# Kernel tuning notes

Hardware: AMD Instinct MI355X
Metric: run time of the kernel (lower is better)

The kernel has to match this reference:

```python
import jax, jax.numpy as jnp
import numpy as np

HIDDEN = 2048
NUM_EXPERTS = 64
TOP_K = 2


def setup_inputs() -> dict:
    key = jax.random.key(0)
    k1, k2 = jax.random.split(key)
    x = jax.random.normal(k1, (4, 4096, HIDDEN), dtype=jnp.float32)
    # nn.Linear(hidden, num_experts, bias=False): weight shape [E, H], y = x @ W.T
    W = jax.random.normal(k2, (NUM_EXPERTS, HIDDEN), dtype=jnp.float32) * (HIDDEN ** -0.5)
    return {"x": x, "W": W}


def reference(x, W):
    B, S, H = x.shape
    E, K = NUM_EXPERTS, TOP_K
    xf = x.reshape(-1, H)                       # [N, H]
    gate_logits = xf @ W.T                      # [N, E]
    routing_probs = jax.nn.softmax(gate_logits, axis=-1)
    top_k_probs, top_k_indices = jax.lax.top_k(routing_probs, K)  # [N, K]
    denom = jnp.sum(top_k_probs, axis=-1, keepdims=True) + 1e-6
    routing_weights = (top_k_probs / denom).reshape(B, S, K)
    expert_indices = top_k_indices.reshape(B, S, K)

    # aux load-balancing loss (training path)
    N = xf.shape[0]
    # expert_mask.mean(0): fraction of tokens assigned to each expert
    assign_per_expert = jnp.zeros((E,), jnp.float32).at[top_k_indices.reshape(-1)].add(1.0) / N
    prob_per_expert = jnp.mean(routing_probs, axis=0)             # [E]
    aux_loss = (jnp.sum(prob_per_expert * prob_per_expert) * E
                + jnp.sum(assign_per_expert * assign_per_expert) * E)

    # expert_counts update (bincount over selected indices)
    expert_counts = jnp.zeros((E,), jnp.float32).at[top_k_indices.reshape(-1)].add(1.0)

    return routing_weights, expert_indices, aux_loss, expert_counts
```

## Files before the change

### kernel.cpp

```cpp
#include <hip/hip_runtime.h>

#define HID 2048
#define NEXP 64
#define NTOK 16384
#define TM 64
#define BK 64
#define NTHREADS 256
#define NCHUNK (HID / BK)
#define RS 72
#define PLANE_B (64 * RS * 2)
#define CHUNK_B (3 * PLANE_B)
#define WS_W_OFF 1024

#define OUT_IDX_OFF (2 * NTOK)
#define OUT_AUX_OFF (4 * NTOK)
#define OUT_CNT_OFF (4 * NTOK + 1)

typedef __attribute__((ext_vector_type(8))) short bhalf8;
typedef __attribute__((ext_vector_type(4))) float f32x4;

__device__ __forceinline__ void split3(float v, unsigned short& h1, unsigned short& h2, unsigned short& h3) {
    unsigned int u = __float_as_uint(v);
    unsigned int r1 = (u + 0x7FFFu + ((u >> 16) & 1u)) & 0xFFFF0000u;
    float f1 = __uint_as_float(r1);
    float d1 = v - f1;
    unsigned int u2 = __float_as_uint(d1);
    unsigned int r2 = (u2 + 0x7FFFu + ((u2 >> 16) & 1u)) & 0xFFFF0000u;
    float f2 = __uint_as_float(r2);
    float d2 = d1 - f2;
    h1 = (unsigned short)(r1 >> 16);
    h2 = (unsigned short)(r2 >> 16);
    h3 = (unsigned short)(__float_as_uint(d2) >> 16);
}

__global__ __launch_bounds__(256) void wsplit_kernel(const float* __restrict__ W, char* __restrict__ wq) {
    int idx8 = (blockIdx.x * 256 + threadIdx.x) * 8;
    int e = idx8 >> 11;
    int kk = idx8 & 2047;
    int c = kk >> 6;
    int j = kk & 63;
    const float4* wp = (const float4*)(W + (size_t)e * HID + kk);
    float4 v0 = wp[0], v1 = wp[1];
    float f[8] = {v0.x, v0.y, v0.z, v0.w, v1.x, v1.y, v1.z, v1.w};
    unsigned int p1[4], p2[4], p3[4];
#pragma unroll
    for (int t = 0; t < 4; t++) {
        unsigned short a1, a2, a3, b1, b2, b3;
        split3(f[2 * t], a1, a2, a3);
        split3(f[2 * t + 1], b1, b2, b3);
        p1[t] = (unsigned int)a1 | ((unsigned int)b1 << 16);
        p2[t] = (unsigned int)a2 | ((unsigned int)b2 << 16);
        p3[t] = (unsigned int)a3 | ((unsigned int)b3 << 16);
    }
    char* base = wq + (size_t)c * CHUNK_B + e * (RS * 2) + j * 2;
    *(uint4*)(base)               = make_uint4(p1[0], p1[1], p1[2], p1[3]);
    *(uint4*)(base + PLANE_B)     = make_uint4(p2[0], p2[1], p2[2], p2[3]);
    *(uint4*)(base + 2 * PLANE_B) = make_uint4(p3[0], p3[1], p3[2], p3[3]);
}

__device__ __forceinline__ void load_x_slot(const float* __restrict__ x, int n0, int c, int s,
                                            float4& a, float4& b) {
    int row = s >> 3, oct = s & 7;
    const float4* gp = (const float4*)(x + (size_t)(n0 + row) * HID + c * BK + oct * 8);
    a = gp[0];
    b = gp[1];
}

__device__ __forceinline__ void conv_store_x(char* xpl, int s, float4 a, float4 b) {
    int row = s >> 3, oct = s & 7;
    float f[8] = {a.x, a.y, a.z, a.w, b.x, b.y, b.z, b.w};
    unsigned int p1[4], p2[4], p3[4];
#pragma unroll
    for (int t = 0; t < 4; t++) {
        unsigned short a1, a2, a3, b1, b2, b3;
        split3(f[2 * t], a1, a2, a3);
        split3(f[2 * t + 1], b1, b2, b3);
        p1[t] = (unsigned int)a1 | ((unsigned int)b1 << 16);
        p2[t] = (unsigned int)a2 | ((unsigned int)b2 << 16);
        p3[t] = (unsigned int)a3 | ((unsigned int)b3 << 16);
    }
    char* base = xpl + row * (RS * 2) + oct * 16;
    *(uint4*)(base)               = make_uint4(p1[0], p1[1], p1[2], p1[3]);
    *(uint4*)(base + PLANE_B)     = make_uint4(p2[0], p2[1], p2[2], p2[3]);
    *(uint4*)(base + 2 * PLANE_B) = make_uint4(p3[0], p3[1], p3[2], p3[3]);
}

__device__ __forceinline__ void dma_w_chunk(const char* gbase, char* lbase, int wave, int lane) {
#pragma unroll
    for (int k = 0; k < 7; k++) {
        int idx = wave + 4 * k;
        if (idx < 27) {
            __builtin_amdgcn_global_load_lds(
                (const __attribute__((address_space(1))) unsigned int*)(gbase + idx * 1024 + lane * 16),
                (__attribute__((address_space(3))) unsigned int*)(lbase + idx * 1024 + lane * 16),
                16, 0, 0);
        }
    }
}

__global__ __launch_bounds__(NTHREADS) void router_main(
    const float* __restrict__ x, const char* __restrict__ wq,
    float* __restrict__ out, float* __restrict__ ws_accum)
{
    __shared__ __align__(16) char xpl[CHUNK_B];
    __shared__ __align__(16) char wpl[2 * CHUNK_B];
    __shared__ float smax[TM];
    __shared__ float sinvZ[TM];
    __shared__ float scount[NEXP];

    const int tid = threadIdx.x;
    const int wave = tid >> 6;
    const int lane = tid & 63;
    const int n0 = blockIdx.x * TM;

    f32x4 acc[4] = {{0.f, 0.f, 0.f, 0.f}, {0.f, 0.f, 0.f, 0.f},
                    {0.f, 0.f, 0.f, 0.f}, {0.f, 0.f, 0.f, 0.f}};

    float4 px0a, px0b, px1a, px1b;

    dma_w_chunk(wq, wpl, wave, lane);
    load_x_slot(x, n0, 0, tid, px0a, px0b);
    load_x_slot(x, n0, 0, tid + NTHREADS, px1a, px1b);

    const int m = lane & 15;
    const int q = lane >> 4;
    const int aBase = (16 * wave + m) * RS + q * 8;

#pragma unroll 1
    for (int c = 0; c < NCHUNK; ++c) {
        const int buf = c & 1;
        conv_store_x(xpl, tid, px0a, px0b);
        conv_store_x(xpl, tid + NTHREADS, px1a, px1b);
        __syncthreads();

        if (c + 1 < NCHUNK) {
            dma_w_chunk(wq + (size_t)(c + 1) * CHUNK_B, wpl + ((c + 1) & 1) * CHUNK_B, wave, lane);
            load_x_slot(x, n0, c + 1, tid, px0a, px0b);
            load_x_slot(x, n0, c + 1, tid + NTHREADS, px1a, px1b);
        }

        const unsigned short* xs = (const unsigned short*)xpl;
        const unsigned short* wb = (const unsigned short*)(wpl + buf * CHUNK_B);

#pragma unroll
        for (int kc = 0; kc < 2; ++kc) {
            const int ka = kc * 32;
            bhalf8 a1 = *(const bhalf8*)(xs + 0 * 4608 + aBase + ka);
            bhalf8 a2 = *(const bhalf8*)(xs + 1 * 4608 + aBase + ka);
            bhalf8 a3 = *(const bhalf8*)(xs + 2 * 4608 + aBase + ka);
#pragma unroll
            for (int t = 0; t < 4; ++t) {
                const int bo = (16 * t + m) * RS + q * 8 + ka;
                bhalf8 b1 = *(const bhalf8*)(wb + 0 * 4608 + bo);
                bhalf8 b2 = *(const bhalf8*)(wb + 1 * 4608 + bo);
                bhalf8 b3 = *(const bhalf8*)(wb + 2 * 4608 + bo);
                acc[t] = __builtin_amdgcn_mfma_f32_16x16x32_bf16(a1, b1, acc[t], 0, 0, 0);
                acc[t] = __builtin_amdgcn_mfma_f32_16x16x32_bf16(a1, b2, acc[t], 0, 0, 0);
                acc[t] = __builtin_amdgcn_mfma_f32_16x16x32_bf16(a2, b1, acc[t], 0, 0, 0);
                acc[t] = __builtin_amdgcn_mfma_f32_16x16x32_bf16(a1, b3, acc[t], 0, 0, 0);
                acc[t] = __builtin_amdgcn_mfma_f32_16x16x32_bf16(a2, b2, acc[t], 0, 0, 0);
                acc[t] = __builtin_amdgcn_mfma_f32_16x16x32_bf16(a3, b1, acc[t], 0, 0, 0);
                acc[t] = __builtin_amdgcn_mfma_f32_16x16x32_bf16(a2, b3, acc[t], 0, 0, 0);
                acc[t] = __builtin_amdgcn_mfma_f32_16x16x32_bf16(a3, b2, acc[t], 0, 0, 0);
                acc[t] = __builtin_amdgcn_mfma_f32_16x16x32_bf16(a3, b3, acc[t], 0, 0, 0);
            }
        }
        __syncthreads();
    }

    float* logits = (float*)xpl;
    {
        const int col = lane & 15;
        const int rbase = (lane >> 4) * 4;
#pragma unroll
        for (int t = 0; t < 4; ++t)
#pragma unroll
            for (int r = 0; r < 4; ++r)
                logits[(16 * wave + rbase + r) * 68 + 16 * t + col] = acc[t][r];
    }
    if (tid < NEXP) scount[tid] = 0.f;
    __syncthreads();

    if (tid < TM) {
        const int t = tid;
        float m1 = -3.4e38f, m2 = -3.4e38f;
        int i1 = 0, i2 = 0;
        for (int e = 0; e < NEXP; e++) {
            float v = logits[t * 68 + e];
            if (v > m1) { m2 = m1; i2 = i1; m1 = v; i1 = e; }
            else if (v > m2) { m2 = v; i2 = e; }
        }
        float Z = 0.f;
        for (int e = 0; e < NEXP; e++)
            Z += __expf(logits[t * 68 + e] - m1);
        float invZ = 1.f / Z;
        float p1 = invZ;
        float p2 = __expf(m2 - m1) * invZ;
        float denom = p1 + p2 + 1e-6f;
        int n = n0 + t;
        out[2 * n + 0] = p1 / denom;
        out[2 * n + 1] = p2 / denom;
        out[OUT_IDX_OFF + 2 * n + 0] = (float)i1;
        out[OUT_IDX_OFF + 2 * n + 1] = (float)i2;
        smax[t] = m1;
        sinvZ[t] = invZ;
        atomicAdd(&scount[i1], 1.f);
        atomicAdd(&scount[i2], 1.f);
    }
    __syncthreads();

    if (tid < NEXP) {
        const int e = tid;
        float s = 0.f;
        for (int t = 0; t < TM; t++)
            s += __expf(logits[t * 68 + e] - smax[t]) * sinvZ[t];
        atomicAdd(&ws_accum[e], s);
        atomicAdd(&ws_accum[NEXP + e], scount[e]);
    }
}

__global__ void router_finish(const float* __restrict__ ws_accum,
                              float* __restrict__ out)
{
    const int e = threadIdx.x;
    const float invN = 1.f / (float)NTOK;
    float p = ws_accum[e] * invN;
    float a = ws_accum[NEXP + e] * invN;
    float v = p * p + a * a;
#pragma unroll
    for (int off = 32; off > 0; off >>= 1)
        v += __shfl_down(v, off);
    if (e == 0) out[OUT_AUX_OFF] = v * (float)NEXP;
    out[OUT_CNT_OFF + e] = ws_accum[NEXP + e];
}

extern "C" void kernel_launch(void* const* d_in, const int* in_sizes, int n_in,
                              void* d_out, int out_size, void* d_ws, size_t ws_size,
                              hipStream_t stream)
{
    const float* x = (const float*)d_in[0];
    const float* W = (const float*)d_in[1];
    float* out = (float*)d_out;
    float* wsf = (float*)d_ws;
    char* wq = (char*)d_ws + WS_W_OFF;

    hipMemsetAsync(wsf, 0, 2 * NEXP * sizeof(float), stream);
    wsplit_kernel<<<64, 256, 0, stream>>>(W, wq);
    router_main<<<NTOK / TM, NTHREADS, 0, stream>>>(x, wq, out, wsf);
    router_finish<<<1, 64, 0, stream>>>(wsf, out);
}
```

Measured before the change: 236.7 us.

## Feed x fragments from registers, halve token tile, split waves over experts

Stops staging x through shared memory. Each lane now loads its own x elements from global memory and splits them into three bf16 MFMA A-fragments in registers. The token tile drops from 64 to 32, with waves split 2x2 over tokens and experts and two accumulators per k-half. This doubles the block count and requests two blocks per CU. The weight buffer is reused for the logits, one barrier per chunk is removed, and the workspace memset is folded into the weight-split kernel. In exchange, each block reads more of W from LDS per token and register pressure rises.

```diff
diff --git a/kernel.cpp b/kernel.cpp
--- a/kernel.cpp
+++ b/kernel.cpp
@@ -3,13 +3,13 @@
 #define HID 2048
 #define NEXP 64
 #define NTOK 16384
-#define TM 64
-#define BK 64
+#define TM 32
 #define NTHREADS 256
-#define NCHUNK (HID / BK)
+#define NCHUNK 32
 #define RS 72
-#define PLANE_B (64 * RS * 2)
-#define CHUNK_B (3 * PLANE_B)
+#define PLANE_S 4608
+#define PLANE_B 9216
+#define CHUNK_B 27648
 #define WS_W_OFF 1024
 
 #define OUT_IDX_OFF (2 * NTOK)
@@ -33,7 +33,25 @@
     h3 = (unsigned short)(__float_as_uint(d2) >> 16);
 }
 
-__global__ __launch_bounds__(256) void wsplit_kernel(const float* __restrict__ W, char* __restrict__ wq) {
+__device__ __forceinline__ void make_frags(float4 va, float4 vb, bhalf8& o1, bhalf8& o2, bhalf8& o3) {
+    float f[8] = {va.x, va.y, va.z, va.w, vb.x, vb.y, vb.z, vb.w};
+    union U { bhalf8 v; unsigned int u[4]; } u1, u2, u3;
+#pragma unroll
+    for (int t = 0; t < 4; t++) {
+        unsigned short a1, a2, a3, b1, b2, b3;
+        split3(f[2 * t], a1, a2, a3);
+        split3(f[2 * t + 1], b1, b2, b3);
+        u1.u[t] = (unsigned int)a1 | ((unsigned int)b1 << 16);
+        u2.u[t] = (unsigned int)a2 | ((unsigned int)b2 << 16);
+        u3.u[t] = (unsigned int)a3 | ((unsigned int)b3 << 16);
+    }
+    o1 = u1.v; o2 = u2.v; o3 = u3.v;
+}
+
+__global__ __launch_bounds__(256) void wsplit_kernel(const float* __restrict__ W,
+                                                     char* __restrict__ wq,
+                                                     float* __restrict__ wsf) {
+    if (blockIdx.x == 0 && threadIdx.x < 2 * NEXP) wsf[threadIdx.x] = 0.f;
     int idx8 = (blockIdx.x * 256 + threadIdx.x) * 8;
     int e = idx8 >> 11;
     int kk = idx8 & 2047;
@@ -58,33 +76,6 @@
     *(uint4*)(base + 2 * PLANE_B) = make_uint4(p3[0], p3[1], p3[2], p3[3]);
 }
 
-__device__ __forceinline__ void load_x_slot(const float* __restrict__ x, int n0, int c, int s,
-                                            float4& a, float4& b) {
-    int row = s >> 3, oct = s & 7;
-    const float4* gp = (const float4*)(x + (size_t)(n0 + row) * HID + c * BK + oct * 8);
-    a = gp[0];
-    b = gp[1];
-}
-
-__device__ __forceinline__ void conv_store_x(char* xpl, int s, float4 a, float4 b) {
-    int row = s >> 3, oct = s & 7;
-    float f[8] = {a.x, a.y, a.z, a.w, b.x, b.y, b.z, b.w};
-    unsigned int p1[4], p2[4], p3[4];
-#pragma unroll
-    for (int t = 0; t < 4; t++) {
-        unsigned short a1, a2, a3, b1, b2, b3;
-        split3(f[2 * t], a1, a2, a3);
-        split3(f[2 * t + 1], b1, b2, b3);
-        p1[t] = (unsigned int)a1 | ((unsigned int)b1 << 16);
-        p2[t] = (unsigned int)a2 | ((unsigned int)b2 << 16);
-        p3[t] = (unsigned int)a3 | ((unsigned int)b3 << 16);
-    }
-    char* base = xpl + row * (RS * 2) + oct * 16;
-    *(uint4*)(base)               = make_uint4(p1[0], p1[1], p1[2], p1[3]);
-    *(uint4*)(base + PLANE_B)     = make_uint4(p2[0], p2[1], p2[2], p2[3]);
-    *(uint4*)(base + 2 * PLANE_B) = make_uint4(p3[0], p3[1], p3[2], p3[3]);
-}
-
 __device__ __forceinline__ void dma_w_chunk(const char* gbase, char* lbase, int wave, int lane) {
 #pragma unroll
     for (int k = 0; k < 7; k++) {
@@ -98,11 +89,10 @@
     }
 }
 
-__global__ __launch_bounds__(NTHREADS) void router_main(
+__global__ __launch_bounds__(NTHREADS, 2) void router_main(
     const float* __restrict__ x, const char* __restrict__ wq,
     float* __restrict__ out, float* __restrict__ ws_accum)
 {
-    __shared__ __align__(16) char xpl[CHUNK_B];
     __shared__ __align__(16) char wpl[2 * CHUNK_B];
     __shared__ float smax[TM];
     __shared__ float sinvZ[TM];
@@ -111,72 +101,76 @@
     const int tid = threadIdx.x;
     const int wave = tid >> 6;
     const int lane = tid & 63;
-    const int n0 = blockIdx.x * TM;
-
-    f32x4 acc[4] = {{0.f, 0.f, 0.f, 0.f}, {0.f, 0.f, 0.f, 0.f},
-                    {0.f, 0.f, 0.f, 0.f}, {0.f, 0.f, 0.f, 0.f}};
-
-    float4 px0a, px0b, px1a, px1b;
-
-    dma_w_chunk(wq, wpl, wave, lane);
-    load_x_slot(x, n0, 0, tid, px0a, px0b);
-    load_x_slot(x, n0, 0, tid + NTHREADS, px1a, px1b);
-
     const int m = lane & 15;
     const int q = lane >> 4;
-    const int aBase = (16 * wave + m) * RS + q * 8;
+    const int tokhalf = wave & 1;
+    const int exphalf = wave >> 1;
+    const int n0 = blockIdx.x * TM;
+
+    const float* xrow = x + (size_t)(n0 + tokhalf * 16 + m) * HID + q * 8;
+
+    f32x4 acc[2][2] = {{{0.f,0.f,0.f,0.f},{0.f,0.f,0.f,0.f}},
+                       {{0.f,0.f,0.f,0.f},{0.f,0.f,0.f,0.f}}};
+
+    dma_w_chunk(wq, wpl, wave, lane);
+    float4 px[2][2];
+    px[0][0] = *(const float4*)(xrow);
+    px[0][1] = *(const float4*)(xrow + 4);
+    px[1][0] = *(const float4*)(xrow + 32);
+    px[1][1] = *(const float4*)(xrow + 36);
 
 #pragma unroll 1
     for (int c = 0; c < NCHUNK; ++c) {
-        const int buf = c & 1;
-        conv_store_x(xpl, tid, px0a, px0b);
-        conv_store_x(xpl, tid + NTHREADS, px1a, px1b);
         __syncthreads();
+        if (c + 1 < NCHUNK)
+            dma_w_chunk(wq + (size_t)(c + 1) * CHUNK_B, wpl + ((c + 1) & 1) * CHUNK_B, wave, lane);
+
+        bhalf8 A[2][3];
+        make_frags(px[0][0], px[0][1], A[0][0], A[0][1], A[0][2]);
+        make_frags(px[1][0], px[1][1], A[1][0], A[1][1], A[1][2]);
 
         if (c + 1 < NCHUNK) {
-            dma_w_chunk(wq + (size_t)(c + 1) * CHUNK_B, wpl + ((c + 1) & 1) * CHUNK_B, wave, lane);
-            load_x_slot(x, n0, c + 1, tid, px0a, px0b);
-            load_x_slot(x, n0, c + 1, tid + NTHREADS, px1a, px1b);
-        }
-
-        const unsigned short* xs = (const unsigned short*)xpl;
-        const unsigned short* wb = (const unsigned short*)(wpl + buf * CHUNK_B);
-
+            const float* xp = xrow + (c + 1) * 64;
+            px[0][0] = *(const float4*)(xp);
+            px[0][1] = *(const float4*)(xp + 4);
+            px[1][0] = *(const float4*)(xp + 32);
+            px[1][1] = *(const float4*)(xp + 36);
+        }
+
+        const unsigned short* wb = (const unsigned short*)(wpl + (c & 1) * CHUNK_B);
 #pragma unroll
         for (int kc = 0; kc < 2; ++kc) {
-            const int ka = kc * 32;
-            bhalf8 a1 = *(const bhalf8*)(xs + 0 * 4608 + aBase + ka);
-            bhalf8 a2 = *(const bhalf8*)(xs + 1 * 4608 + aBase + ka);
-            bhalf8 a3 = *(const bhalf8*)(xs + 2 * 4608 + aBase + ka);
-#pragma unroll
-            for (int t = 0; t < 4; ++t) {
-                const int bo = (16 * t + m) * RS + q * 8 + ka;
-                bhalf8 b1 = *(const bhalf8*)(wb + 0 * 4608 + bo);
-                bhalf8 b2 = *(const bhalf8*)(wb + 1 * 4608 + bo);
-                bhalf8 b3 = *(const bhalf8*)(wb + 2 * 4608 + bo);
-                acc[t] = __builtin_amdgcn_mfma_f32_16x16x32_bf16(a1, b1, acc[t], 0, 0, 0);
-                acc[t] = __builtin_amdgcn_mfma_f32_16x16x32_bf16(a1, b2, acc[t], 0, 0, 0);
-                acc[t] = __builtin_amdgcn_mfma_f32_16x16x32_bf16(a2, b1, acc[t], 0, 0, 0);
-                acc[t] = __builtin_amdgcn_mfma_f32_16x16x32_bf16(a1, b3, acc[t], 0, 0, 0);
-                acc[t] = __builtin_amdgcn_mfma_f32_16x16x32_bf16(a2, b2, acc[t], 0, 0, 0);
-                acc[t] = __builtin_amdgcn_mfma_f32_16x16x32_bf16(a3, b1, acc[t], 0, 0, 0);
-                acc[t] = __builtin_amdgcn_mfma_f32_16x16x32_bf16(a2, b3, acc[t], 0, 0, 0);
-                acc[t] = __builtin_amdgcn_mfma_f32_16x16x32_bf16(a3, b2, acc[t], 0, 0, 0);
-                acc[t] = __builtin_amdgcn_mfma_f32_16x16x32_bf16(a3, b3, acc[t], 0, 0, 0);
+#pragma unroll
+            for (int t = 0; t < 2; ++t) {
+                const int bo = (exphalf * 32 + t * 16 + m) * RS + kc * 32 + q * 8;
+                bhalf8 b1 = *(const bhalf8*)(wb + 0 * PLANE_S + bo);
+                bhalf8 b2 = *(const bhalf8*)(wb + 1 * PLANE_S + bo);
+                bhalf8 b3 = *(const bhalf8*)(wb + 2 * PLANE_S + bo);
+                f32x4 a4 = acc[t][kc];
+                a4 = __builtin_amdgcn_mfma_f32_16x16x32_bf16(A[kc][0], b1, a4, 0, 0, 0);
+                a4 = __builtin_amdgcn_mfma_f32_16x16x32_bf16(A[kc][0], b2, a4, 0, 0, 0);
+                a4 = __builtin_amdgcn_mfma_f32_16x16x32_bf16(A[kc][1], b1, a4, 0, 0, 0);
+                a4 = __builtin_amdgcn_mfma_f32_16x16x32_bf16(A[kc][0], b3, a4, 0, 0, 0);
+                a4 = __builtin_amdgcn_mfma_f32_16x16x32_bf16(A[kc][1], b2, a4, 0, 0, 0);
+                a4 = __builtin_amdgcn_mfma_f32_16x16x32_bf16(A[kc][2], b1, a4, 0, 0, 0);
+                a4 = __builtin_amdgcn_mfma_f32_16x16x32_bf16(A[kc][1], b3, a4, 0, 0, 0);
+                a4 = __builtin_amdgcn_mfma_f32_16x16x32_bf16(A[kc][2], b2, a4, 0, 0, 0);
+                a4 = __builtin_amdgcn_mfma_f32_16x16x32_bf16(A[kc][2], b3, a4, 0, 0, 0);
+                acc[t][kc] = a4;
             }
         }
-        __syncthreads();
-    }
-
-    float* logits = (float*)xpl;
+    }
+
+    float* logits = (float*)wpl;
     {
         const int col = lane & 15;
         const int rbase = (lane >> 4) * 4;
 #pragma unroll
-        for (int t = 0; t < 4; ++t)
+        for (int t = 0; t < 2; ++t)
 #pragma unroll
             for (int r = 0; r < 4; ++r)
-                logits[(16 * wave + rbase + r) * 68 + 16 * t + col] = acc[t][r];
+                logits[(tokhalf * 16 + rbase + r) * 68 + exphalf * 32 + t * 16 + col] =
+                    acc[t][0][r] + acc[t][1][r];
     }
     if (tid < NEXP) scount[tid] = 0.f;
     __syncthreads();
@@ -244,8 +238,7 @@
     float* wsf = (float*)d_ws;
     char* wq = (char*)d_ws + WS_W_OFF;
 
-    hipMemsetAsync(wsf, 0, 2 * NEXP * sizeof(float), stream);
-    wsplit_kernel<<<64, 256, 0, stream>>>(W, wq);
+    wsplit_kernel<<<64, 256, 0, stream>>>(W, wq, wsf);
     router_main<<<NTOK / TM, NTHREADS, 0, stream>>>(x, wq, out, wsf);
     router_finish<<<1, 64, 0, stream>>>(wsf, out);
 }
```

New measurement: 236.2 us. About the same (-0.2%).
